# Kernel optimization log

Hardware: AMD Instinct MI355X
Metric: run time of the kernel (lower is better)

The kernel has to match this reference:

```python
import jax, jax.numpy as jnp
import numpy as np

B, S, D = 2, 2048, 2048
H, KV, HD = 32, 8, 64  # num_heads, num_kv_heads, head_dim
NREP = H // KV


def rotate_half(x):
    x1, x2 = x[..., : x.shape[-1] // 2], x[..., x.shape[-1] // 2 :]
    return jnp.concatenate((-x2, x1), axis=-1)


def setup_inputs() -> dict:
    key = jax.random.key(0)
    ks = jax.random.split(key, 5)
    x = jax.random.normal(ks[0], (B, S, D), dtype=jnp.float32)
    # weights stored as [in, out] so y = x @ W (same math as nn.Linear with random init)
    Wq = jax.random.normal(ks[1], (D, D), dtype=jnp.float32) * (D ** -0.5)
    Wk = jax.random.normal(ks[2], (D, KV * HD), dtype=jnp.float32) * (D ** -0.5)
    Wv = jax.random.normal(ks[3], (D, KV * HD), dtype=jnp.float32) * (D ** -0.5)
    Wo = jax.random.normal(ks[4], (D, D), dtype=jnp.float32) * (D ** -0.5)
    # standard RoPE tables, broadcastable over [B, H, S, HD]
    inv_freq = 1.0 / (10000.0 ** (jnp.arange(0, HD, 2, dtype=jnp.float32) / HD))
    freqs = jnp.arange(S, dtype=jnp.float32)[:, None] * inv_freq[None, :]  # [S, HD/2]
    emb = jnp.concatenate((freqs, freqs), axis=-1)  # [S, HD]
    cos = jnp.cos(emb)[None, None]  # [1,1,S,HD]
    sin = jnp.sin(emb)[None, None]
    # causal mask, masked where == 0
    attention_mask = jnp.tril(jnp.ones((S, S), dtype=jnp.int32))[None, None]
    return {"x": x, "cos": cos, "sin": sin, "Wq": Wq, "Wk": Wk, "Wv": Wv,
            "Wo": Wo, "attention_mask": attention_mask}


def reference(x, cos, sin, Wq, Wk, Wv, Wo, attention_mask):
    b, s, _ = x.shape
    q = (x @ Wq).reshape(b, s, H, HD).transpose(0, 2, 1, 3)   # [B,H,S,HD]
    k = (x @ Wk).reshape(b, s, KV, HD).transpose(0, 2, 1, 3)  # [B,KV,S,HD]
    v = (x @ Wv).reshape(b, s, KV, HD).transpose(0, 2, 1, 3)  # [B,KV,S,HD]
    # RoPE (elementwise) commutes with head-repeat; apply before grouping
    q = q * cos + rotate_half(q) * sin
    k = k * cos + rotate_half(k) * sin
    # GQA head broadcast instead of repeat_interleave: group q as [B,KV,NREP,S,HD]
    qg = q.reshape(b, KV, NREP, s, HD)
    scores = jnp.einsum('bgrqd,bgkd->bgrqk', qg, k) / jnp.sqrt(jnp.float32(HD))
    scores = jnp.where(attention_mask[:, :, None] == 0, jnp.float32(-1e9), scores)
    probs = jax.nn.softmax(scores, axis=-1)
    out = jnp.einsum('bgrqk,bgkd->bgrqd', probs, v)           # [B,KV,NREP,S,HD]
    out = out.reshape(b, H, s, HD).transpose(0, 2, 1, 3).reshape(b, s, H * HD)
    return out @ Wo
```

## Files before the change

kernel.cpp:

```cpp
#include <hip/hip_runtime.h>
#include <hip/hip_bf16.h>
#include <stdint.h>

#define B_ 2
#define S_ 2048
#define D_ 2048
#define H_ 32
#define KV_ 8
#define HD_ 64
#define NQKV 3072

typedef __bf16 bf16_t;
typedef __bf16 bf16x8 __attribute__((ext_vector_type(8)));
typedef __bf16 bf16x4 __attribute__((ext_vector_type(4)));
typedef float  f32x4  __attribute__((ext_vector_type(4)));
typedef float  f32x16 __attribute__((ext_vector_type(16)));
typedef unsigned int u32;
typedef u32 u32x4 __attribute__((ext_vector_type(4)));

typedef const __attribute__((address_space(1))) uint32_t* gp1_t;
typedef __attribute__((address_space(3))) uint32_t* lp3_t;

__device__ inline void gload_lds16(const void* g, void* l) {
  __builtin_amdgcn_global_load_lds((gp1_t)(uintptr_t)g, (lp3_t)(uint32_t)(uintptr_t)l,
                                   16, 0, 0);
}

__device__ inline u32 pkbf(float a, float b) {
  union { bf16_t h[2]; u32 u; } v;
  v.h[0] = (bf16_t)a; v.h[1] = (bf16_t)b;
  return v.u;
}

__device__ inline void pl32swap(u32 &a, u32 &b) {
  asm("v_permlane32_swap_b32 %0, %1" : "+v"(a), "+v"(b));
}

__global__ void cvt_f32_bf16(const float* __restrict__ in, bf16_t* __restrict__ out, int n4) {
  int i = blockIdx.x * blockDim.x + threadIdx.x;
  if (i < n4) {
    float4 v = ((const float4*)in)[i];
    bf16x4 o;
    o[0] = (bf16_t)v.x; o[1] = (bf16_t)v.y; o[2] = (bf16_t)v.z; o[3] = (bf16_t)v.w;
    ((bf16x4*)out)[i] = o;
  }
}

__global__ void transpose_cvt(const float* __restrict__ in, bf16_t* __restrict__ out,
                              int C, int row_off) {
  __shared__ float t[32][33];
  int tx = threadIdx.x, ty = threadIdx.y;
  int c0 = blockIdx.x * 32, r0 = blockIdx.y * 32;
#pragma unroll
  for (int j = 0; j < 4; ++j)
    t[ty + j*8][tx] = in[(int64_t)(r0 + ty + j*8) * C + c0 + tx];
  __syncthreads();
#pragma unroll
  for (int j = 0; j < 4; ++j)
    out[(int64_t)(row_off + c0 + ty + j*8) * 2048 + r0 + tx] = (bf16_t)t[tx][ty + j*8];
}

__global__ void v_transpose(const bf16_t* __restrict__ Vbuf, bf16_t* __restrict__ Vt) {
  __shared__ bf16_t t[32][34];
  const int tx = threadIdx.x, ty = threadIdx.y;
  const int c0 = blockIdx.x * 32;
  const int s0 = blockIdx.y * 32;
  const int b  = blockIdx.z;
#pragma unroll
  for (int j = 0; j < 4; ++j)
    t[ty + j*8][tx] = Vbuf[(int64_t)(b * S_ + s0 + ty + j*8) * 512 + c0 + tx];
  __syncthreads();
#pragma unroll
  for (int j = 0; j < 4; ++j)
    Vt[(int64_t)(b * 512 + c0 + ty + j*8) * S_ + s0 + tx] = t[tx][ty + j*8];
}

#define QSCALE 0.18033688011112042f
template <int BN, int EPI>
__global__ __launch_bounds__(512, 2) void gemm256(const bf16_t* __restrict__ A,
                                                  const bf16_t* __restrict__ Bt,
                                                  const float* __restrict__ cosb,
                                                  const float* __restrict__ sinb,
                                                  bf16_t* __restrict__ Q,
                                                  bf16_t* __restrict__ Kr,
                                                  bf16_t* __restrict__ Vbuf,
                                                  float* __restrict__ Cout,
                                                  int N, int K) {
  constexpr int NB = BN / 64;
  constexpr int LT = 4 + NB;
  constexpr int WCOLS = BN / 4;
  constexpr int NF = WCOLS / 16;
  constexpr int NHALF = NF / 2;

  __shared__ bf16_t As[2][256 * 64];
  __shared__ bf16_t Bs[2][BN * 64];

  const int tid = threadIdx.x;
  const int w = tid >> 6, lane = tid & 63;
  const int l15 = lane & 15, l4 = lane >> 4;
  const int wr = w >> 2, wc = w & 3;
  const int bm = blockIdx.y * 256, bn = blockIdx.x * BN;

  const int rw = w * 8 + (lane >> 3);
  const int srcg = ((lane & 7) ^ ((lane >> 3) & 7)) << 3;
  const bf16_t* PA[4];
  const bf16_t* PB[NB];
#pragma unroll
  for (int L = 0; L < 4; ++L)
    PA[L] = A + (int64_t)(bm + L * 64 + rw) * K + srcg;
#pragma unroll
  for (int L = 0; L < NB; ++L)
    PB[L] = Bt + (int64_t)(bn + L * 64 + rw) * K + srcg;

  const int NK = K >> 6;
  const int xr = l15 & 7;
  const int g0 = (l4 ^ xr) << 3;
  const int g1 = ((4 + l4) ^ xr) << 3;

  f32x4 acc[8][NF] = {};

#pragma unroll
  for (int s = 0; s < LT; ++s) {
    if (s < 4) gload_lds16(PA[s], &As[0][s * 4096 + w * 512]);
    else       gload_lds16(PB[s - 4], &Bs[0][(s - 4) * 4096 + w * 512]);
  }
  asm volatile("s_waitcnt vmcnt(0)" ::: "memory");
  __syncthreads();

  for (int t = 0; t < NK; ++t) {
    const int p = t & 1;
    const bool more = (t + 1) < NK;
    const int toff = (t + 1) << 6;
    const bf16_t* Ab = &As[p][0];
    const bf16_t* Bb = &Bs[p][0];
#pragma unroll
    for (int q = 0; q < 4; ++q) {
      if (q < 2 && more) {
        const int s0 = q * (LT / 2), s1 = s0 + LT / 2;
#pragma unroll
        for (int s = s0; s < s1; ++s) {
          if (s < 4) gload_lds16(PA[s] + toff, &As[p ^ 1][s * 4096 + w * 512]);
          else       gload_lds16(PB[s - 4] + toff, &Bs[p ^ 1][(s - 4) * 4096 + w * 512]);
        }
      }
      const int mh = q >> 1, nh = q & 1;
      bf16x8 af[4][2], bfv[NHALF][2];
#pragma unroll
      for (int mm = 0; mm < 4; ++mm) {
        const int ra = wr * 128 + (mh * 4 + mm) * 16 + l15;
        af[mm][0] = *(const bf16x8*)(Ab + ra * 64 + g0);
        af[mm][1] = *(const bf16x8*)(Ab + ra * 64 + g1);
      }
#pragma unroll
      for (int nn = 0; nn < NHALF; ++nn) {
        const int rb = wc * WCOLS + (nh * NHALF + nn) * 16 + l15;
        bfv[nn][0] = *(const bf16x8*)(Bb + rb * 64 + g0);
        bfv[nn][1] = *(const bf16x8*)(Bb + rb * 64 + g1);
      }
      __builtin_amdgcn_s_setprio(1);
#pragma unroll
      for (int mm = 0; mm < 4; ++mm)
#pragma unroll
        for (int nn = 0; nn < NHALF; ++nn) {
          acc[mh*4+mm][nh*NHALF+nn] = __builtin_amdgcn_mfma_f32_16x16x32_bf16(
              af[mm][0], bfv[nn][0], acc[mh*4+mm][nh*NHALF+nn], 0, 0, 0);
          acc[mh*4+mm][nh*NHALF+nn] = __builtin_amdgcn_mfma_f32_16x16x32_bf16(
              af[mm][1], bfv[nn][1], acc[mh*4+mm][nh*NHALF+nn], 0, 0, 0);
        }
      __builtin_amdgcn_s_setprio(0);
    }
    if (more) {
      asm volatile("s_waitcnt vmcnt(0)" ::: "memory");
      __syncthreads();
    }
  }

  if constexpr (EPI == 0) {
#pragma unroll
    for (int m = 0; m < 8; ++m) {
      const int row = bm + wr * 128 + m * 16 + l4 * 4;
#pragma unroll
      for (int n = 0; n < NF; ++n) {
        const int col = bn + wc * WCOLS + n * 16 + l15;
#pragma unroll
        for (int r = 0; r < 4; ++r)
          Cout[(int64_t)(row + r) * N + col] = acc[m][n][r];
      }
    }
  } else {
    const int colbase = bn + wc * 64;
    if (colbase < 2048) {
      const int h = colbase >> 6;
#pragma unroll
      for (int m = 0; m < 8; ++m) {
#pragma unroll
        for (int r = 0; r < 4; ++r) {
          const int srow = bm + wr * 128 + m * 16 + l4 * 4 + r;
          const int b = srow >> 11, s = srow & 2047;
          const float* cs = cosb + s * HD_;
          const float* sn = sinb + s * HD_;
          bf16_t* qp = Q + ((int64_t)(b * H_ + h) * S_ + s) * HD_;
#pragma unroll
          for (int n = 0; n < 4; ++n) {
            const int d = n * 16 + l15;
            const float sgn = (n & 2) ? 1.f : -1.f;
            float o = (acc[m][n][r] * cs[d] + sgn * acc[m][n ^ 2][r] * sn[d]) * QSCALE;
            qp[d] = (bf16_t)o;
          }
        }
      }
    } else if (colbase < 2560) {
      const int kvh = (colbase - 2048) >> 6;
#pragma unroll
      for (int m = 0; m < 8; ++m) {
#pragma unroll
        for (int r = 0; r < 4; ++r) {
          const int srow = bm + wr * 128 + m * 16 + l4 * 4 + r;
          const int b = srow >> 11, s = srow & 2047;
          const float* cs = cosb + s * HD_;
          const float* sn = sinb + s * HD_;
          bf16_t* kp = Kr + ((int64_t)(b * KV_ + kvh) * S_ + s) * HD_;
#pragma unroll
          for (int n = 0; n < 4; ++n) {
            const int d = n * 16 + l15;
            const float sgn = (n & 2) ? 1.f : -1.f;
            float o = acc[m][n][r] * cs[d] + sgn * acc[m][n ^ 2][r] * sn[d];
            kp[d] = (bf16_t)o;
          }
        }
      }
    } else {
      const int ccb = colbase - 2560;
#pragma unroll
      for (int m = 0; m < 8; ++m) {
#pragma unroll
        for (int r = 0; r < 4; ++r) {
          const int srow = bm + wr * 128 + m * 16 + l4 * 4 + r;
          bf16_t* vp = Vbuf + (int64_t)srow * 512 + ccb;
#pragma unroll
          for (int n = 0; n < 4; ++n)
            vp[n * 16 + l15] = (bf16_t)acc[m][n][r];
        }
      }
    }
  }
}

#define SHIFT_ 8.0f
__global__ __launch_bounds__(512, 2) void attn5(const bf16_t* __restrict__ Q,
                                                const bf16_t* __restrict__ Kr,
                                                const bf16_t* __restrict__ Vt,
                                                bf16_t* __restrict__ AO) {
  const int bk = blockIdx.x;
  const int b = bk >> 3, kvh = bk & 7;
  const int qc = 31 - (int)blockIdx.y;
  const int tid = threadIdx.x;
  const int w = tid >> 6, lane = tid & 63;
  const int l31 = lane & 31, hi = lane >> 5;
  const int h = kvh * 4 + (w & 3);
  const int q0w = qc * 64 + (w >> 2) * 32;

  __shared__ __align__(16) bf16_t Ks[2][64 * 64];
  __shared__ __align__(16) bf16_t Vs[2][64 * 64];

  const bf16_t* Qb = Q  + ((int64_t)(b * H_ + h) * S_ + q0w) * HD_;
  const bf16_t* Kg = Kr + (int64_t)(b * KV_ + kvh) * S_ * HD_;
  const bf16_t* Vg = Vt + (int64_t)(b * KV_ + kvh) * HD_ * S_;

  const int rL = (w << 3) + (lane >> 3);
  const int sgr = ((lane & 7) ^ (rL & 7)) << 3;
  const bf16_t* Ksrc = Kg + rL * HD_ + sgr;
  const bf16_t* Vsrc = Vg + (int64_t)rL * S_ + sgr;
  char* KsDst = (char*)&Ks[0][0] + w * 1024;
  char* VsDst = (char*)&Vs[0][0] + w * 1024;

  bf16x8 qf[4];
#pragma unroll
  for (int ds = 0; ds < 4; ++ds)
    qf[ds] = *(const bf16x8*)(Qb + l31 * HD_ + ds * 16 + hi * 8);

  f32x16 accO0 = {}, accO1 = {};
  float lhalf = 0.f;
  const int NT = qc + 1;
  const int xorb = l31 & 7;

  const char* KsB = (const char*)&Ks[0][0];
  const char* VsB = (const char*)&Vs[0][0];

  gload_lds16(Ksrc, KsDst);
  gload_lds16(Vsrc, VsDst);
  asm volatile("s_waitcnt vmcnt(0)" ::: "memory");
  __syncthreads();

  for (int t = 0; t < NT; ++t) {
    const int cur = t & 1;
    if (t + 1 < NT) {
      gload_lds16(Ksrc + (t + 1) * 64 * HD_, KsDst + (cur ^ 1) * 8192);
      gload_lds16(Vsrc + (t + 1) * 64,      VsDst + (cur ^ 1) * 8192);
    }
#pragma unroll
    for (int sub = 0; sub < 2; ++sub) {
      const int kvbase = t * 64 + sub * 32;
      if (kvbase <= q0w) {
        const bool diag = (kvbase == q0w);
        const char* Kbase = KsB + cur * 8192 + (sub * 32 + l31) * 128;
        f32x16 sacc = {};
        __builtin_amdgcn_s_setprio(1);
#pragma unroll
        for (int ds = 0; ds < 4; ++ds) {
          bf16x8 kf = *(const bf16x8*)(Kbase + ((((ds << 1) + hi) ^ xorb) << 4));
          sacc = __builtin_amdgcn_mfma_f32_32x32x16_bf16(kf, qf[ds], sacc, 0, 0, 0);
        }
        __builtin_amdgcn_s_setprio(0);
        float p[16];
#pragma unroll
        for (int r = 0; r < 16; ++r) {
          float sc = sacc[r];
          if (diag) {
            int kvpos = (r & 3) + 8 * (r >> 2) + 4 * hi;
            if (kvpos > l31) sc = -1e30f;
          }
          p[r] = __builtin_amdgcn_exp2f(sc - SHIFT_);
        }
        float t0 = (p[0] + p[1]) + (p[2] + p[3]);
        float t1 = (p[4] + p[5]) + (p[6] + p[7]);
        float t2 = (p[8] + p[9]) + (p[10] + p[11]);
        float t3 = (p[12] + p[13]) + (p[14] + p[15]);
        lhalf += (t0 + t1) + (t2 + t3);
        u32 pk[8];
#pragma unroll
        for (int i = 0; i < 8; ++i) pk[i] = pkbf(p[2*i], p[2*i+1]);
        u32 a0 = pk[0], b0 = pk[2]; pl32swap(a0, b0);
        u32 a1 = pk[1], b1 = pk[3]; pl32swap(a1, b1);
        u32 a2 = pk[4], b2 = pk[6]; pl32swap(a2, b2);
        u32 a3 = pk[5], b3 = pk[7]; pl32swap(a3, b3);
        bf16x8 pf0 = __builtin_bit_cast(bf16x8, (u32x4){a0, a1, b0, b1});
        bf16x8 pf1 = __builtin_bit_cast(bf16x8, (u32x4){a2, a3, b2, b3});
        const char* Vb0 = VsB + cur * 8192 + l31 * 128;
        const char* Vb1 = VsB + cur * 8192 + (32 + l31) * 128;
        const int c0 = (sub << 2) + hi;
        const int c1 = (sub << 2) + 2 + hi;
        bf16x8 v00 = *(const bf16x8*)(Vb0 + ((c0 ^ xorb) << 4));
        bf16x8 v01 = *(const bf16x8*)(Vb0 + ((c1 ^ xorb) << 4));
        bf16x8 v10 = *(const bf16x8*)(Vb1 + ((c0 ^ xorb) << 4));
        bf16x8 v11 = *(const bf16x8*)(Vb1 + ((c1 ^ xorb) << 4));
        __builtin_amdgcn_s_setprio(1);
        accO0 = __builtin_amdgcn_mfma_f32_32x32x16_bf16(v00, pf0, accO0, 0, 0, 0);
        accO1 = __builtin_amdgcn_mfma_f32_32x32x16_bf16(v10, pf0, accO1, 0, 0, 0);
        accO0 = __builtin_amdgcn_mfma_f32_32x32x16_bf16(v01, pf1, accO0, 0, 0, 0);
        accO1 = __builtin_amdgcn_mfma_f32_32x32x16_bf16(v11, pf1, accO1, 0, 0, 0);
        __builtin_amdgcn_s_setprio(0);
      }
    }
    asm volatile("s_waitcnt vmcnt(0)" ::: "memory");
    __syncthreads();
  }

  float lrun = lhalf + __shfl_xor(lhalf, 32);
  const float rl = 1.f / lrun;
  const int64_t row = (int64_t)(b * S_ + q0w + l31);
#pragma unroll
  for (int dt = 0; dt < 2; ++dt) {
#pragma unroll
    for (int g = 0; g < 4; ++g) {
      bf16x4 ov;
#pragma unroll
      for (int j = 0; j < 4; ++j) {
        float val = (dt ? accO1[4*g + j] : accO0[4*g + j]) * rl;
        ov[j] = (bf16_t)val;
      }
      const int d0 = dt * 32 + g * 8 + hi * 4;
      *(bf16x4*)(AO + row * D_ + h * HD_ + d0) = ov;
    }
  }
}

extern "C" void kernel_launch(void* const* d_in, const int* in_sizes, int n_in,
                              void* d_out, int out_size, void* d_ws, size_t ws_size,
                              hipStream_t stream) {
  const float* x    = (const float*)d_in[0];
  const float* cosb = (const float*)d_in[1];
  const float* sinb = (const float*)d_in[2];
  const float* Wq   = (const float*)d_in[3];
  const float* Wk   = (const float*)d_in[4];
  const float* Wv   = (const float*)d_in[5];
  const float* Wo   = (const float*)d_in[6];
  float* out = (float*)d_out;

  bf16_t* ws = (bf16_t*)d_ws;
  size_t o = 0;
  bf16_t* xb    = ws + o; o += (size_t)4096 * 2048;
  bf16_t* Wqkvt = ws + o; o += (size_t)3072 * 2048;
  bf16_t* Wot   = ws + o; o += (size_t)2048 * 2048;
  bf16_t* Qr    = ws + o; o += (size_t)B_ * H_ * S_ * HD_;
  bf16_t* Krb   = ws + o; o += (size_t)B_ * KV_ * S_ * HD_;
  bf16_t* Vtb   = ws + o; o += (size_t)B_ * KV_ * S_ * HD_;
  bf16_t* Vbuf  = ws + o; o += (size_t)B_ * S_ * 512;
  bf16_t* AO    = ws + o; o += (size_t)4096 * 2048;

  cvt_f32_bf16<<<(8388608/4 + 255)/256, 256, 0, stream>>>(x, xb, 8388608/4);
  transpose_cvt<<<dim3(2048/32, 2048/32), dim3(32, 8), 0, stream>>>(Wq, Wqkvt, 2048, 0);
  transpose_cvt<<<dim3(512/32, 2048/32),  dim3(32, 8), 0, stream>>>(Wk, Wqkvt, 512, 2048);
  transpose_cvt<<<dim3(512/32, 2048/32),  dim3(32, 8), 0, stream>>>(Wv, Wqkvt, 512, 2560);
  transpose_cvt<<<dim3(2048/32, 2048/32), dim3(32, 8), 0, stream>>>(Wo, Wot, 2048, 0);
  gemm256<256, 1><<<dim3(3072/256, 4096/256), 512, 0, stream>>>(
      xb, Wqkvt, cosb, sinb, Qr, Krb, Vbuf, nullptr, 3072, 2048);
  v_transpose<<<dim3(16, 64, 2), dim3(32, 8), 0, stream>>>(Vbuf, Vtb);
  attn5<<<dim3(16, 32), 512, 0, stream>>>(Qr, Krb, Vtb, AO);
  gemm256<128, 0><<<dim3(2048/128, 4096/256), 512, 0, stream>>>(
      AO, Wot, nullptr, nullptr, nullptr, nullptr, nullptr, out, 2048, 2048);
}
```

Before: 190.4 us.

## Triple-buffer attention K/V loads and hoist GEMM B fragments per k-step

The attention kernel moves from double to triple buffering of K/V tiles. It issues two tiles ahead and waits with vmcnt(2) at the top of each iteration, which removes the full drain and barrier at the end of each step. The softmax shift is folded into the score accumulator's initial value, dropping a subtract per element, and the launch-bounds min-blocks hint is removed. In the GEMM, B fragments are loaded once per k-step for all columns instead of per quarter, which cuts LDS reads but raises register pressure and may reduce occupancy.

```diff
diff --git a/kernel.cpp b/kernel.cpp
--- a/kernel.cpp
+++ b/kernel.cpp
@@ -90,7 +90,6 @@
   constexpr int LT = 4 + NB;
   constexpr int WCOLS = BN / 4;
   constexpr int NF = WCOLS / 16;
-  constexpr int NHALF = NF / 2;
 
   __shared__ bf16_t As[2][256 * 64];
   __shared__ bf16_t Bs[2][BN * 64];
@@ -133,39 +132,41 @@
     const int toff = (t + 1) << 6;
     const bf16_t* Ab = &As[p][0];
     const bf16_t* Bb = &Bs[p][0];
-#pragma unroll
-    for (int q = 0; q < 4; ++q) {
-      if (q < 2 && more) {
-        const int s0 = q * (LT / 2), s1 = s0 + LT / 2;
+
+    bf16x8 ball[NF][2];
+#pragma unroll
+    for (int nn = 0; nn < NF; ++nn) {
+      const int rb = wc * WCOLS + nn * 16 + l15;
+      ball[nn][0] = *(const bf16x8*)(Bb + rb * 64 + g0);
+      ball[nn][1] = *(const bf16x8*)(Bb + rb * 64 + g1);
+    }
+
+#pragma unroll
+    for (int mh = 0; mh < 2; ++mh) {
+      if (more) {
+        const int s0 = mh * (LT / 2), s1 = s0 + LT / 2;
 #pragma unroll
         for (int s = s0; s < s1; ++s) {
           if (s < 4) gload_lds16(PA[s] + toff, &As[p ^ 1][s * 4096 + w * 512]);
           else       gload_lds16(PB[s - 4] + toff, &Bs[p ^ 1][(s - 4) * 4096 + w * 512]);
         }
       }
-      const int mh = q >> 1, nh = q & 1;
-      bf16x8 af[4][2], bfv[NHALF][2];
+      bf16x8 af[4][2];
 #pragma unroll
       for (int mm = 0; mm < 4; ++mm) {
         const int ra = wr * 128 + (mh * 4 + mm) * 16 + l15;
         af[mm][0] = *(const bf16x8*)(Ab + ra * 64 + g0);
         af[mm][1] = *(const bf16x8*)(Ab + ra * 64 + g1);
       }
-#pragma unroll
-      for (int nn = 0; nn < NHALF; ++nn) {
-        const int rb = wc * WCOLS + (nh * NHALF + nn) * 16 + l15;
-        bfv[nn][0] = *(const bf16x8*)(Bb + rb * 64 + g0);
-        bfv[nn][1] = *(const bf16x8*)(Bb + rb * 64 + g1);
-      }
       __builtin_amdgcn_s_setprio(1);
 #pragma unroll
       for (int mm = 0; mm < 4; ++mm)
 #pragma unroll
-        for (int nn = 0; nn < NHALF; ++nn) {
-          acc[mh*4+mm][nh*NHALF+nn] = __builtin_amdgcn_mfma_f32_16x16x32_bf16(
-              af[mm][0], bfv[nn][0], acc[mh*4+mm][nh*NHALF+nn], 0, 0, 0);
-          acc[mh*4+mm][nh*NHALF+nn] = __builtin_amdgcn_mfma_f32_16x16x32_bf16(
-              af[mm][1], bfv[nn][1], acc[mh*4+mm][nh*NHALF+nn], 0, 0, 0);
+        for (int nn = 0; nn < NF; ++nn) {
+          acc[mh*4+mm][nn] = __builtin_amdgcn_mfma_f32_16x16x32_bf16(
+              af[mm][0], ball[nn][0], acc[mh*4+mm][nn], 0, 0, 0);
+          acc[mh*4+mm][nn] = __builtin_amdgcn_mfma_f32_16x16x32_bf16(
+              af[mm][1], ball[nn][1], acc[mh*4+mm][nn], 0, 0, 0);
         }
       __builtin_amdgcn_s_setprio(0);
     }
@@ -247,10 +248,10 @@
 }
 
 #define SHIFT_ 8.0f
-__global__ __launch_bounds__(512, 2) void attn5(const bf16_t* __restrict__ Q,
-                                                const bf16_t* __restrict__ Kr,
-                                                const bf16_t* __restrict__ Vt,
-                                                bf16_t* __restrict__ AO) {
+__global__ __launch_bounds__(512) void attn6(const bf16_t* __restrict__ Q,
+                                             const bf16_t* __restrict__ Kr,
+                                             const bf16_t* __restrict__ Vt,
+                                             bf16_t* __restrict__ AO) {
   const int bk = blockIdx.x;
   const int b = bk >> 3, kvh = bk & 7;
   const int qc = 31 - (int)blockIdx.y;
@@ -260,8 +261,8 @@
   const int h = kvh * 4 + (w & 3);
   const int q0w = qc * 64 + (w >> 2) * 32;
 
-  __shared__ __align__(16) bf16_t Ks[2][64 * 64];
-  __shared__ __align__(16) bf16_t Vs[2][64 * 64];
+  __shared__ __align__(16) bf16_t Ks[3][64 * 64];
+  __shared__ __align__(16) bf16_t Vs[3][64 * 64];
 
   const bf16_t* Qb = Q  + ((int64_t)(b * H_ + h) * S_ + q0w) * HD_;
   const bf16_t* Kg = Kr + (int64_t)(b * KV_ + kvh) * S_ * HD_;
@@ -274,6 +275,15 @@
   char* KsDst = (char*)&Ks[0][0] + w * 1024;
   char* VsDst = (char*)&Vs[0][0] + w * 1024;
 
+  const int NT = qc + 1;
+
+  auto stage = [&](int t) {
+    const int tc = (t < NT) ? t : (NT - 1);
+    const int bufo = (t % 3) * 8192;
+    gload_lds16(Ksrc + tc * 64 * HD_, KsDst + bufo);
+    gload_lds16(Vsrc + tc * 64,      VsDst + bufo);
+  };
+
   bf16x8 qf[4];
 #pragma unroll
   for (int ds = 0; ds < 4; ++ds)
@@ -281,30 +291,31 @@
 
   f32x16 accO0 = {}, accO1 = {};
   float lhalf = 0.f;
-  const int NT = qc + 1;
   const int xorb = l31 & 7;
 
   const char* KsB = (const char*)&Ks[0][0];
   const char* VsB = (const char*)&Vs[0][0];
 
-  gload_lds16(Ksrc, KsDst);
-  gload_lds16(Vsrc, VsDst);
-  asm volatile("s_waitcnt vmcnt(0)" ::: "memory");
-  __syncthreads();
+  const f32x16 sinit = {SHIFT_ > 0 ? -SHIFT_ : 0.f, -SHIFT_, -SHIFT_, -SHIFT_,
+                        -SHIFT_, -SHIFT_, -SHIFT_, -SHIFT_,
+                        -SHIFT_, -SHIFT_, -SHIFT_, -SHIFT_,
+                        -SHIFT_, -SHIFT_, -SHIFT_, -SHIFT_};
+
+  stage(0);
+  stage(1);
 
   for (int t = 0; t < NT; ++t) {
-    const int cur = t & 1;
-    if (t + 1 < NT) {
-      gload_lds16(Ksrc + (t + 1) * 64 * HD_, KsDst + (cur ^ 1) * 8192);
-      gload_lds16(Vsrc + (t + 1) * 64,      VsDst + (cur ^ 1) * 8192);
-    }
+    asm volatile("s_waitcnt vmcnt(2)" ::: "memory");
+    __syncthreads();
+    stage(t + 2);
+    const int curo = (t % 3) * 8192;
 #pragma unroll
     for (int sub = 0; sub < 2; ++sub) {
       const int kvbase = t * 64 + sub * 32;
       if (kvbase <= q0w) {
         const bool diag = (kvbase == q0w);
-        const char* Kbase = KsB + cur * 8192 + (sub * 32 + l31) * 128;
-        f32x16 sacc = {};
+        const char* Kbase = KsB + curo + (sub * 32 + l31) * 128;
+        f32x16 sacc = sinit;
         __builtin_amdgcn_s_setprio(1);
 #pragma unroll
         for (int ds = 0; ds < 4; ++ds) {
@@ -320,7 +331,7 @@
             int kvpos = (r & 3) + 8 * (r >> 2) + 4 * hi;
             if (kvpos > l31) sc = -1e30f;
           }
-          p[r] = __builtin_amdgcn_exp2f(sc - SHIFT_);
+          p[r] = __builtin_amdgcn_exp2f(sc);
         }
         float t0 = (p[0] + p[1]) + (p[2] + p[3]);
         float t1 = (p[4] + p[5]) + (p[6] + p[7]);
@@ -336,8 +347,8 @@
         u32 a3 = pk[5], b3 = pk[7]; pl32swap(a3, b3);
         bf16x8 pf0 = __builtin_bit_cast(bf16x8, (u32x4){a0, a1, b0, b1});
         bf16x8 pf1 = __builtin_bit_cast(bf16x8, (u32x4){a2, a3, b2, b3});
-        const char* Vb0 = VsB + cur * 8192 + l31 * 128;
-        const char* Vb1 = VsB + cur * 8192 + (32 + l31) * 128;
+        const char* Vb0 = VsB + curo + l31 * 128;
+        const char* Vb1 = VsB + curo + (32 + l31) * 128;
         const int c0 = (sub << 2) + hi;
         const int c1 = (sub << 2) + 2 + hi;
         bf16x8 v00 = *(const bf16x8*)(Vb0 + ((c0 ^ xorb) << 4));
@@ -352,9 +363,9 @@
         __builtin_amdgcn_s_setprio(0);
       }
     }
-    asm volatile("s_waitcnt vmcnt(0)" ::: "memory");
-    __syncthreads();
-  }
+  }
+
+  asm volatile("s_waitcnt vmcnt(0)" ::: "memory");
 
   float lrun = lhalf + __shfl_xor(lhalf, 32);
   const float rl = 1.f / lrun;
@@ -406,7 +417,7 @@
   gemm256<256, 1><<<dim3(3072/256, 4096/256), 512, 0, stream>>>(
       xb, Wqkvt, cosb, sinb, Qr, Krb, Vbuf, nullptr, 3072, 2048);
   v_transpose<<<dim3(16, 64, 2), dim3(32, 8), 0, stream>>>(Vbuf, Vtb);
-  attn5<<<dim3(16, 32), 512, 0, stream>>>(Qr, Krb, Vtb, AO);
+  attn6<<<dim3(16, 32), 512, 0, stream>>>(Qr, Krb, Vtb, AO);
   gemm256<128, 0><<<dim3(2048/128, 4096/256), 512, 0, stream>>>(
       AO, Wot, nullptr, nullptr, nullptr, nullptr, nullptr, out, 2048, 2048);
 }
```

Result: no change. 187.2 us (-1.7%).
